# Performance work log

Measured on AMD Instinct MI355X. Metric: run time of the kernel, lower is better.

## Reference

```python
import jax, jax.numpy as jnp
import numpy as np
from jax import lax
from jax.scipy.special import logsumexp

NUM_TAGS = 5
B, L = 16384, 512


def setup_inputs() -> dict:
    key = jax.random.key(0)
    k1, k2, k3, k4, k5 = jax.random.split(key, 5)
    emissions = jax.random.normal(k1, (B, L, NUM_TAGS), dtype=jnp.float32)
    tags = jax.random.randint(k2, (B, L), 0, NUM_TAGS)
    mask = jnp.ones((B, L), dtype=bool)
    # learned CRF parameters, init U(-0.1, 0.1) as in reset_parameters
    transitions = jax.random.uniform(k3, (NUM_TAGS, NUM_TAGS), minval=-0.1, maxval=0.1, dtype=jnp.float32)
    start_transitions = jax.random.uniform(k4, (NUM_TAGS,), minval=-0.1, maxval=0.1, dtype=jnp.float32)
    end_transitions = jax.random.uniform(k5, (NUM_TAGS,), minval=-0.1, maxval=0.1, dtype=jnp.float32)
    return {
        "emissions": emissions,
        "transitions": transitions,
        "start_transitions": start_transitions,
        "end_transitions": end_transitions,
        "tags": tags,
        "mask": mask,
    }


def reference(emissions, transitions, start_transitions, end_transitions, tags, mask):
    """CRF mean negative log-likelihood: log_partition - gold_score (both batch means)."""
    Bs, Ls, C = emissions.shape
    maskf = mask.astype(emissions.dtype)

    # ---- log partition (forward algorithm); note: original torch code's
    # mask application here is a no-op (where(mask, s, s)), reproduced faithfully.
    init_score = start_transitions[None, :] + emissions[:, 0]  # (B, C)

    def step(score, em_i):
        # score: (B, C) over previous tag; em_i: (B, C)
        nxt = logsumexp(score[:, :, None] + transitions[None, :, :] + em_i[:, None, :], axis=1)
        return nxt, None

    ems = jnp.swapaxes(emissions[:, 1:], 0, 1)  # (L-1, B, C)
    final_score, _ = lax.scan(step, init_score, ems)
    log_den = logsumexp(final_score + end_transitions[None, :], axis=1).mean()

    # ---- gold path score (fully vectorized over time)
    s0 = start_transitions[tags[:, 0]] + jnp.take_along_axis(emissions[:, 0], tags[:, :1], axis=1)[:, 0]
    trans_scores = transitions[tags[:, :-1], tags[:, 1:]]  # (B, L-1)
    em_at_tags = jnp.take_along_axis(emissions, tags[:, :, None], axis=2)[:, :, 0]  # (B, L)
    path_score = s0 + ((trans_scores + em_at_tags[:, 1:]) * maskf[:, 1:]).sum(axis=1)
    last_idx = mask.sum(axis=1).astype(jnp.int32) - 1  # (B,)
    last_tags = jnp.take_along_axis(tags, last_idx[:, None], axis=1)[:, 0]
    log_num = (path_score + end_transitions[last_tags]).mean()

    return log_den - log_num
```

## Files before the change

### kernel.cpp

```cpp
#include <hip/hip_runtime.h>

#define NTAGS 5
#define BATCH 16384
#define SEQL 512
#define CL 8
#define SEQF (SEQL * NTAGS)
#define PADC 41
#define SEQPF (64 * PADC)
#define PTAG 9
#define SEQPT (64 * PTAG)

__device__ __forceinline__ float sel5v(float a0, float a1, float a2, float a3, float a4, int t) {
    float r = a0;
    r = (t == 1) ? a1 : r;
    r = (t == 2) ? a2 : r;
    r = (t == 3) ? a3 : r;
    r = (t == 4) ? a4 : r;
    return r;
}

__global__ __launch_bounds__(256, 2) void crf_fused(
    const float* __restrict__ emis, const float* __restrict__ trans,
    const float* __restrict__ startT, const float* __restrict__ endT,
    const int* __restrict__ tags, float* __restrict__ out) {
    __shared__ float lemis[4 * SEQPF];
    __shared__ int ltags[4 * SEQPT];
    __shared__ float ldsT[25];
    __shared__ float lred[4];

    const int tid = threadIdx.x;
    const int lane = tid & 63;
    const int wid = tid >> 6;

    const float4* ge = (const float4*)(emis + (size_t)blockIdx.x * 4 * SEQF);
#pragma unroll
    for (int w = 0; w < 10; ++w) {
        const int f = w * 256 + tid;
        const float4 v = ge[f];
        const int F = 4 * f;
        const int s = F / SEQF;
        const int r = F - s * SEQF;
        const int piece = r / 40;
        const int off = r - piece * 40;
        float* dst = &lemis[s * SEQPF + piece * PADC + off];
        dst[0] = v.x; dst[1] = v.y; dst[2] = v.z; dst[3] = v.w;
    }
    const int4* gt4 = (const int4*)(tags + (size_t)blockIdx.x * 4 * SEQL);
#pragma unroll
    for (int w = 0; w < 2; ++w) {
        const int g = w * 256 + tid;
        const int4 v = gt4[g];
        const int T = 4 * g;
        const int s = T >> 9;
        const int q = T & 511;
        const int piece = q >> 3;
        const int j = q & 7;
        int* dst = &ltags[s * SEQPT + piece * PTAG + j];
        dst[0] = v.x; dst[1] = v.y; dst[2] = v.z; dst[3] = v.w;
    }
    if (tid < 25) ldsT[tid] = trans[tid];
    __syncthreads();

    float eT[25];
#pragma unroll
    for (int i = 0; i < 25; ++i) eT[i] = __expf(trans[i]);

    const float* E = &lemis[wid * SEQPF + lane * PADC];
    const int* G = &ltags[wid * SEQPT + lane * PTAG];

    float M[25];
#pragma unroll
    for (int i = 0; i < 25; ++i) M[i] = 0.f;
    M[0] = M[6] = M[12] = M[18] = M[24] = 1.f;
    float logS = 0.f, path = 0.f;
    int prev = (lane == 0) ? 0 : G[7 - PTAG];

#pragma unroll
    for (int t = 0; t < CL; ++t) {
        const float e0 = E[t * 5 + 0], e1 = E[t * 5 + 1], e2 = E[t * 5 + 2],
                    e3 = E[t * 5 + 3], e4 = E[t * 5 + 4];
        const int tag = G[t];
        if (lane == 0 && t == 0) {
            path += sel5v(startT[0], startT[1], startT[2], startT[3], startT[4], tag) +
                    sel5v(e0, e1, e2, e3, e4, tag);
            prev = tag;
        } else {
            const float ex0 = __expf(e0), ex1 = __expf(e1), ex2 = __expf(e2),
                        ex3 = __expf(e3), ex4 = __expf(e4);
#pragma unroll
            for (int i = 0; i < 5; ++i) {
                const float m0 = M[i * 5 + 0], m1 = M[i * 5 + 1], m2 = M[i * 5 + 2],
                            m3 = M[i * 5 + 3], m4 = M[i * 5 + 4];
#pragma unroll
                for (int j = 0; j < 5; ++j) {
                    float a = m0 * eT[j];
                    a = fmaf(m1, eT[5 + j], a);
                    a = fmaf(m2, eT[10 + j], a);
                    a = fmaf(m3, eT[15 + j], a);
                    a = fmaf(m4, eT[20 + j], a);
                    const float exj = (j == 0) ? ex0 : (j == 1) ? ex1 : (j == 2) ? ex2
                                     : (j == 3) ? ex3 : ex4;
                    M[i * 5 + j] = a * exj;
                }
            }
            path += ldsT[prev * 5 + tag] + sel5v(e0, e1, e2, e3, e4, tag);
            prev = tag;
        }
        if ((t & 3) == 3) {
            float m = M[0];
#pragma unroll
            for (int i = 1; i < 25; ++i) m = fmaxf(m, M[i]);
            logS += __logf(m);
            const float rc = __builtin_amdgcn_rcpf(m);
#pragma unroll
            for (int i = 0; i < 25; ++i) M[i] *= rc;
        }
    }

#pragma unroll
    for (int lvl = 0; lvl < 6; ++lvl) {
        const int mk = 1 << lvl;
        float O[25];
#pragma unroll
        for (int i = 0; i < 25; ++i) O[i] = __shfl_xor(M[i], mk, 64);
        const float oS = __shfl_xor(logS, mk, 64);
        const bool hi = (lane & mk) != 0;
        float L[25], R[25];
#pragma unroll
        for (int i = 0; i < 25; ++i) {
            L[i] = hi ? O[i] : M[i];
            R[i] = hi ? M[i] : O[i];
        }
        float NM[25];
#pragma unroll
        for (int i = 0; i < 5; ++i)
#pragma unroll
            for (int j = 0; j < 5; ++j) {
                float a = L[i * 5 + 0] * R[0 * 5 + j];
                a = fmaf(L[i * 5 + 1], R[1 * 5 + j], a);
                a = fmaf(L[i * 5 + 2], R[2 * 5 + j], a);
                a = fmaf(L[i * 5 + 3], R[3 * 5 + j], a);
                a = fmaf(L[i * 5 + 4], R[4 * 5 + j], a);
                NM[i * 5 + j] = a;
            }
        logS += oS;
        float mx = NM[0];
#pragma unroll
        for (int i = 1; i < 25; ++i) mx = fmaxf(mx, NM[i]);
        logS += __logf(mx);
        const float rc = __builtin_amdgcn_rcpf(mx);
#pragma unroll
        for (int i = 0; i < 25; ++i) M[i] = NM[i] * rc;
    }

#pragma unroll
    for (int o = 1; o < 64; o <<= 1) path += __shfl_xor(path, o, 64);

    const float* E0 = &lemis[wid * SEQPF];
    const float s0 = startT[0] + E0[0], s1 = startT[1] + E0[1], s2 = startT[2] + E0[2],
                s3 = startT[3] + E0[3], s4 = startT[4] + E0[4];
    const float m0 = fmaxf(fmaxf(fmaxf(s0, s1), fmaxf(s2, s3)), s4);
    const float v0 = __expf(s0 - m0), v1 = __expf(s1 - m0), v2 = __expf(s2 - m0),
                v3 = __expf(s3 - m0), v4 = __expf(s4 - m0);
    float nv[5];
#pragma unroll
    for (int j = 0; j < 5; ++j) {
        float a = v0 * M[0 * 5 + j];
        a = fmaf(v1, M[1 * 5 + j], a);
        a = fmaf(v2, M[2 * 5 + j], a);
        a = fmaf(v3, M[3 * 5 + j], a);
        a = fmaf(v4, M[4 * 5 + j], a);
        nv[j] = a;
    }
    const float en0 = endT[0], en1 = endT[1], en2 = endT[2], en3 = endT[3], en4 = endT[4];
    float sden = nv[0] * __expf(en0);
    sden = fmaf(nv[1], __expf(en1), sden);
    sden = fmaf(nv[2], __expf(en2), sden);
    sden = fmaf(nv[3], __expf(en3), sden);
    sden = fmaf(nv[4], __expf(en4), sden);
    const float den = m0 + logS + __logf(sden);

    const int lastTag = ltags[wid * SEQPT + 63 * PTAG + 7];
    const float num = path + sel5v(en0, en1, en2, en3, en4, lastTag);

    const float res = (den - num) * (1.0f / (float)BATCH);
    if (lane == 0) lred[wid] = res;
    __syncthreads();
    if (tid == 0) atomicAdd(out, lred[0] + lred[1] + lred[2] + lred[3]);
}

extern "C" void kernel_launch(void* const* d_in, const int* in_sizes, int n_in,
                              void* d_out, int out_size, void* d_ws, size_t ws_size,
                              hipStream_t stream) {
    const float* emis = (const float*)d_in[0];
    const float* trans = (const float*)d_in[1];
    const float* startT = (const float*)d_in[2];
    const float* endT = (const float*)d_in[3];
    const int* tags = (const int*)d_in[4];
    float* out = (float*)d_out;

    hipMemsetAsync(out, 0, sizeof(float), stream);
    crf_fused<<<dim3(BATCH / 4), dim3(256), 0, stream>>>(emis, trans, startT, endT, tags,
                                                         out);
}
```

Baseline: 307.0 us.

## Split CRF into chunk-matrix phase and per-sequence vector combine phase

The in-wave 6-level butterfly of 5x5 matrix products is cut to 2 levels. Each group of 4 lanes writes its 5x5 transfer matrix, log scale and partial path score to a workspace, and a second kernel folds the 16 records per sequence with cheap vector-matrix products. Phase 1 also drops the first-step identity multiply by seeding M directly, normalises once instead of every 4 steps, and computes the gold path score in a separate loop. This removes most of the 125-FMA matrix-matrix products and shuffles at the cost of a workspace round trip through global memory and a second launch. Skipping normalisation inside the chunk and between the two butterfly levels risks overflow or underflow.

New measurement: 296.4 us. -3.4%, faster.

```diff
diff --git a/kernel.cpp b/kernel.cpp
--- a/kernel.cpp
+++ b/kernel.cpp
@@ -9,6 +9,8 @@
 #define SEQPF (64 * PADC)
 #define PTAG 9
 #define SEQPT (64 * PTAG)
+#define NREC 16
+#define RECF 28
 
 __device__ __forceinline__ float sel5v(float a0, float a1, float a2, float a3, float a4, int t) {
     float r = a0;
@@ -18,15 +20,17 @@
     r = (t == 4) ? a4 : r;
     return r;
 }
-
-__global__ __launch_bounds__(256, 2) void crf_fused(
+__device__ __forceinline__ float f4c(float4 v, int c) {
+    switch (c & 3) { case 0: return v.x; case 1: return v.y; case 2: return v.z; default: return v.w; }
+}
+
+__global__ __launch_bounds__(256, 2) void crf_phase1(
     const float* __restrict__ emis, const float* __restrict__ trans,
-    const float* __restrict__ startT, const float* __restrict__ endT,
-    const int* __restrict__ tags, float* __restrict__ out) {
+    const float* __restrict__ startT, const int* __restrict__ tags,
+    float* __restrict__ ws) {
     __shared__ float lemis[4 * SEQPF];
     __shared__ int ltags[4 * SEQPT];
     __shared__ float ldsT[25];
-    __shared__ float lred[4];
 
     const int tid = threadIdx.x;
     const int lane = tid & 63;
@@ -64,29 +68,50 @@
     float eT[25];
 #pragma unroll
     for (int i = 0; i < 25; ++i) eT[i] = __expf(trans[i]);
+    float stR[5];
+#pragma unroll
+    for (int j = 0; j < 5; ++j) stR[j] = startT[j];
 
     const float* E = &lemis[wid * SEQPF + lane * PADC];
     const int* G = &ltags[wid * SEQPT + lane * PTAG];
 
+    float path = 0.f;
+    int prev = (lane == 0) ? 0 : G[7 - PTAG];
+#pragma unroll
+    for (int t = 0; t < CL; ++t) {
+        const int tag = G[t];
+        const float et = E[t * 5 + tag];
+        if (lane == 0 && t == 0) {
+            path += sel5v(stR[0], stR[1], stR[2], stR[3], stR[4], tag) + et;
+        } else {
+            path += ldsT[prev * 5 + tag] + et;
+        }
+        prev = tag;
+    }
+
     float M[25];
-#pragma unroll
-    for (int i = 0; i < 25; ++i) M[i] = 0.f;
-    M[0] = M[6] = M[12] = M[18] = M[24] = 1.f;
-    float logS = 0.f, path = 0.f;
-    int prev = (lane == 0) ? 0 : G[7 - PTAG];
-
-#pragma unroll
-    for (int t = 0; t < CL; ++t) {
-        const float e0 = E[t * 5 + 0], e1 = E[t * 5 + 1], e2 = E[t * 5 + 2],
-                    e3 = E[t * 5 + 3], e4 = E[t * 5 + 4];
-        const int tag = G[t];
-        if (lane == 0 && t == 0) {
-            path += sel5v(startT[0], startT[1], startT[2], startT[3], startT[4], tag) +
-                    sel5v(e0, e1, e2, e3, e4, tag);
-            prev = tag;
-        } else {
-            const float ex0 = __expf(e0), ex1 = __expf(e1), ex2 = __expf(e2),
-                        ex3 = __expf(e3), ex4 = __expf(e4);
+    float logS = 0.f;
+    const int bump = (lane == 0) ? 1 : 0;
+    {
+        const float* e = &E[bump * 5];
+        const float x0 = __expf(e[0]), x1 = __expf(e[1]), x2 = __expf(e[2]),
+                    x3 = __expf(e[3]), x4 = __expf(e[4]);
+#pragma unroll
+        for (int i = 0; i < 5; ++i) {
+            M[i * 5 + 0] = eT[i * 5 + 0] * x0;
+            M[i * 5 + 1] = eT[i * 5 + 1] * x1;
+            M[i * 5 + 2] = eT[i * 5 + 2] * x2;
+            M[i * 5 + 3] = eT[i * 5 + 3] * x3;
+            M[i * 5 + 4] = eT[i * 5 + 4] * x4;
+        }
+    }
+#pragma unroll
+    for (int u = 1; u < CL; ++u) {
+        const int s = u + bump;
+        if (s < CL) {
+            const float* e = &E[s * 5];
+            const float ex0 = __expf(e[0]), ex1 = __expf(e[1]), ex2 = __expf(e[2]),
+                        ex3 = __expf(e[3]), ex4 = __expf(e[4]);
 #pragma unroll
             for (int i = 0; i < 5; ++i) {
                 const float m0 = M[i * 5 + 0], m1 = M[i * 5 + 1], m2 = M[i * 5 + 2],
@@ -103,22 +128,20 @@
                     M[i * 5 + j] = a * exj;
                 }
             }
-            path += ldsT[prev * 5 + tag] + sel5v(e0, e1, e2, e3, e4, tag);
-            prev = tag;
-        }
-        if ((t & 3) == 3) {
-            float m = M[0];
-#pragma unroll
-            for (int i = 1; i < 25; ++i) m = fmaxf(m, M[i]);
-            logS += __logf(m);
-            const float rc = __builtin_amdgcn_rcpf(m);
-#pragma unroll
-            for (int i = 0; i < 25; ++i) M[i] *= rc;
-        }
-    }
-
-#pragma unroll
-    for (int lvl = 0; lvl < 6; ++lvl) {
+        }
+    }
+    {
+        float mx = M[0];
+#pragma unroll
+        for (int i = 1; i < 25; ++i) mx = fmaxf(mx, M[i]);
+        logS += __logf(mx);
+        const float rc = __builtin_amdgcn_rcpf(mx);
+#pragma unroll
+        for (int i = 0; i < 25; ++i) M[i] *= rc;
+    }
+
+#pragma unroll
+    for (int lvl = 0; lvl < 2; ++lvl) {
         const int mk = 1 << lvl;
         float O[25];
 #pragma unroll
@@ -131,7 +154,6 @@
             L[i] = hi ? O[i] : M[i];
             R[i] = hi ? M[i] : O[i];
         }
-        float NM[25];
 #pragma unroll
         for (int i = 0; i < 5; ++i)
 #pragma unroll
@@ -141,52 +163,118 @@
                 a = fmaf(L[i * 5 + 2], R[2 * 5 + j], a);
                 a = fmaf(L[i * 5 + 3], R[3 * 5 + j], a);
                 a = fmaf(L[i * 5 + 4], R[4 * 5 + j], a);
-                NM[i * 5 + j] = a;
+                M[i * 5 + j] = a;
             }
         logS += oS;
-        float mx = NM[0];
-#pragma unroll
-        for (int i = 1; i < 25; ++i) mx = fmaxf(mx, NM[i]);
+    }
+    {
+        float mx = M[0];
+#pragma unroll
+        for (int i = 1; i < 25; ++i) mx = fmaxf(mx, M[i]);
         logS += __logf(mx);
         const float rc = __builtin_amdgcn_rcpf(mx);
 #pragma unroll
-        for (int i = 0; i < 25; ++i) M[i] = NM[i] * rc;
-    }
-
-#pragma unroll
-    for (int o = 1; o < 64; o <<= 1) path += __shfl_xor(path, o, 64);
-
-    const float* E0 = &lemis[wid * SEQPF];
-    const float s0 = startT[0] + E0[0], s1 = startT[1] + E0[1], s2 = startT[2] + E0[2],
-                s3 = startT[3] + E0[3], s4 = startT[4] + E0[4];
+        for (int i = 0; i < 25; ++i) M[i] *= rc;
+    }
+    path += __shfl_xor(path, 1, 64);
+    path += __shfl_xor(path, 2, 64);
+
+    float* rb = &lemis[wid * SEQPF];
+    if ((lane & 3) == 0) {
+        float* r = &rb[(lane >> 2) * RECF];
+#pragma unroll
+        for (int i = 0; i < 25; ++i) r[i] = M[i];
+        r[25] = logS;
+        r[26] = path;
+        r[27] = 0.f;
+    }
+    __syncthreads();
+    float4* wdst = (float4*)(ws + (size_t)blockIdx.x * (4 * NREC * RECF));
+    {
+        const int F = 4 * tid;
+        const int s = F / 448;
+        const int r = F - s * 448;
+        wdst[tid] = *(const float4*)&lemis[s * SEQPF + r];
+        if (tid < 192) {
+            const int k = 256 + tid;
+            const int F2 = 4 * k;
+            const int s2 = F2 / 448;
+            const int r2 = F2 - s2 * 448;
+            wdst[k] = *(const float4*)&lemis[s2 * SEQPF + r2];
+        }
+    }
+}
+
+__device__ __forceinline__ void p2_combine(const float4 r[7], float v[5], float& logZ,
+                                           float& path) {
+#define MM(i, j) f4c(r[((i) * 5 + (j)) >> 2], ((i) * 5 + (j)) & 3)
+    float nv[5];
+#pragma unroll
+    for (int j = 0; j < 5; ++j) {
+        float a = v[0] * MM(0, j);
+        a = fmaf(v[1], MM(1, j), a);
+        a = fmaf(v[2], MM(2, j), a);
+        a = fmaf(v[3], MM(3, j), a);
+        a = fmaf(v[4], MM(4, j), a);
+        nv[j] = a;
+    }
+#undef MM
+    logZ += r[6].y;
+    path += r[6].z;
+    const float m = fmaxf(fmaxf(fmaxf(nv[0], nv[1]), fmaxf(nv[2], nv[3])), nv[4]);
+    logZ += __logf(m);
+    const float rc = __builtin_amdgcn_rcpf(m);
+#pragma unroll
+    for (int j = 0; j < 5; ++j) v[j] = nv[j] * rc;
+}
+
+__global__ __launch_bounds__(64) void crf_phase2(
+    const float* __restrict__ emis, const float* __restrict__ startT,
+    const float* __restrict__ endT, const int* __restrict__ tags,
+    const float* __restrict__ ws, float* __restrict__ out) {
+    const int seq = blockIdx.x * 64 + threadIdx.x;
+    const float* eb = emis + (size_t)seq * (SEQL * NTAGS);
+    const float4* wsb = (const float4*)(ws + (size_t)seq * NREC * RECF);
+
+    float4 r[4][7];
+#pragma unroll
+    for (int s = 0; s < 4; ++s)
+#pragma unroll
+        for (int k = 0; k < 7; ++k) r[s][k] = wsb[s * 7 + k];
+
+    const float4 e03 = *(const float4*)eb;
+    const float e4v = eb[4];
+    const float s0 = startT[0] + e03.x, s1 = startT[1] + e03.y, s2 = startT[2] + e03.z,
+                s3 = startT[3] + e03.w, s4 = startT[4] + e4v;
     const float m0 = fmaxf(fmaxf(fmaxf(s0, s1), fmaxf(s2, s3)), s4);
-    const float v0 = __expf(s0 - m0), v1 = __expf(s1 - m0), v2 = __expf(s2 - m0),
-                v3 = __expf(s3 - m0), v4 = __expf(s4 - m0);
-    float nv[5];
-#pragma unroll
-    for (int j = 0; j < 5; ++j) {
-        float a = v0 * M[0 * 5 + j];
-        a = fmaf(v1, M[1 * 5 + j], a);
-        a = fmaf(v2, M[2 * 5 + j], a);
-        a = fmaf(v3, M[3 * 5 + j], a);
-        a = fmaf(v4, M[4 * 5 + j], a);
-        nv[j] = a;
-    }
+    float v[5] = {__expf(s0 - m0), __expf(s1 - m0), __expf(s2 - m0), __expf(s3 - m0),
+                  __expf(s4 - m0)};
+    float logZ = m0, path = 0.f;
+
+#pragma unroll
+    for (int c = 0; c < NREC; ++c) {
+        p2_combine(r[c & 3], v, logZ, path);
+        if (c + 4 < NREC) {
+#pragma unroll
+            for (int k = 0; k < 7; ++k) r[c & 3][k] = wsb[(c + 4) * 7 + k];
+        }
+    }
+
     const float en0 = endT[0], en1 = endT[1], en2 = endT[2], en3 = endT[3], en4 = endT[4];
-    float sden = nv[0] * __expf(en0);
-    sden = fmaf(nv[1], __expf(en1), sden);
-    sden = fmaf(nv[2], __expf(en2), sden);
-    sden = fmaf(nv[3], __expf(en3), sden);
-    sden = fmaf(nv[4], __expf(en4), sden);
-    const float den = m0 + logS + __logf(sden);
-
-    const int lastTag = ltags[wid * SEQPT + 63 * PTAG + 7];
+    float sden = v[0] * __expf(en0);
+    sden = fmaf(v[1], __expf(en1), sden);
+    sden = fmaf(v[2], __expf(en2), sden);
+    sden = fmaf(v[3], __expf(en3), sden);
+    sden = fmaf(v[4], __expf(en4), sden);
+    const float den = logZ + __logf(sden);
+
+    const int lastTag = tags[seq * SEQL + (SEQL - 1)];
     const float num = path + sel5v(en0, en1, en2, en3, en4, lastTag);
 
-    const float res = (den - num) * (1.0f / (float)BATCH);
-    if (lane == 0) lred[wid] = res;
-    __syncthreads();
-    if (tid == 0) atomicAdd(out, lred[0] + lred[1] + lred[2] + lred[3]);
+    float val = (den - num) * (1.0f / (float)BATCH);
+#pragma unroll
+    for (int off = 32; off > 0; off >>= 1) val += __shfl_xor(val, off, 64);
+    if (threadIdx.x == 0) atomicAdd(out, val);
 }
 
 extern "C" void kernel_launch(void* const* d_in, const int* in_sizes, int n_in,
@@ -198,8 +286,10 @@
     const float* endT = (const float*)d_in[3];
     const int* tags = (const int*)d_in[4];
     float* out = (float*)d_out;
+    float* ws = (float*)d_ws;
 
     hipMemsetAsync(out, 0, sizeof(float), stream);
-    crf_fused<<<dim3(BATCH / 4), dim3(256), 0, stream>>>(emis, trans, startT, endT, tags,
-                                                         out);
-}
+    crf_phase1<<<dim3(BATCH / 4), dim3(256), 0, stream>>>(emis, trans, startT, tags, ws);
+    crf_phase2<<<dim3(BATCH / 64), dim3(64), 0, stream>>>(emis, startT, endT, tags, ws,
+                                                          out);
+}
```

## Replace per-lane 5x5 matrix scan with forward-backward vector recurrences per sequence

Applied to the files above, without the earlier changes.

Each sequence was split into 64 chunks, each lane built a 5x5 transfer matrix with 25-element products, and the chunks were combined by a shuffle tree. The new kernel gives one thread a whole sequence half: wave 0 runs the forward recurrence over the first 256 steps and wave 1 runs the backward recurrence over the last 256. Both carry only 5-element vectors and meet at the middle through LDS. This cuts per-step arithmetic roughly fivefold and removes the matrix-combine tree. In exchange, each thread's serial chain now spans 256 steps. To hide load latency, emissions and tags are staged in 16-step windows with register prefetch and LDS double buffering, and the grid drops to 256 blocks of 128 threads, which may leave the GPU's compute units underused.

New measurement: 283.2 us. 7.8% less time.

```diff
diff --git a/kernel.cpp b/kernel.cpp
--- a/kernel.cpp
+++ b/kernel.cpp
@@ -3,12 +3,10 @@
 #define NTAGS 5
 #define BATCH 16384
 #define SEQL 512
-#define CL 8
-#define SEQF (SEQL * NTAGS)
-#define PADC 41
-#define SEQPF (64 * PADC)
-#define PTAG 9
-#define SEQPT (64 * PTAG)
+#define TW 16
+#define NW 16
+#define ROWF 81
+#define ROWT 17
 
 __device__ __forceinline__ float sel5v(float a0, float a1, float a2, float a3, float a4, int t) {
     float r = a0;
@@ -19,174 +17,201 @@
     return r;
 }
 
-__global__ __launch_bounds__(256, 2) void crf_fused(
+__global__ __launch_bounds__(128, 1) void crf_fb(
     const float* __restrict__ emis, const float* __restrict__ trans,
     const float* __restrict__ startT, const float* __restrict__ endT,
     const int* __restrict__ tags, float* __restrict__ out) {
-    __shared__ float lemis[4 * SEQPF];
-    __shared__ int ltags[4 * SEQPT];
+    __shared__ float lem[2][128 * ROWF];
+    __shared__ int ltg[2][128 * ROWT];
     __shared__ float ldsT[25];
-    __shared__ float lred[4];
+    __shared__ float xch[64][9];
 
     const int tid = threadIdx.x;
-    const int lane = tid & 63;
-    const int wid = tid >> 6;
-
-    const float4* ge = (const float4*)(emis + (size_t)blockIdx.x * 4 * SEQF);
-#pragma unroll
-    for (int w = 0; w < 10; ++w) {
-        const int f = w * 256 + tid;
-        const float4 v = ge[f];
-        const int F = 4 * f;
-        const int s = F / SEQF;
-        const int r = F - s * SEQF;
-        const int piece = r / 40;
-        const int off = r - piece * 40;
-        float* dst = &lemis[s * SEQPF + piece * PADC + off];
-        dst[0] = v.x; dst[1] = v.y; dst[2] = v.z; dst[3] = v.w;
-    }
-    const int4* gt4 = (const int4*)(tags + (size_t)blockIdx.x * 4 * SEQL);
-#pragma unroll
-    for (int w = 0; w < 2; ++w) {
-        const int g = w * 256 + tid;
-        const int4 v = gt4[g];
-        const int T = 4 * g;
-        const int s = T >> 9;
-        const int q = T & 511;
-        const int piece = q >> 3;
-        const int j = q & 7;
-        int* dst = &ltags[s * SEQPT + piece * PTAG + j];
-        dst[0] = v.x; dst[1] = v.y; dst[2] = v.z; dst[3] = v.w;
-    }
-    if (tid < 25) ldsT[tid] = trans[tid];
+    const int l = tid & 63;
+    const int wv = tid >> 6;
+    const int seqbase = blockIdx.x * 64;
+    const int lrow = wv * 64 + l;
+
+    if (l < 25) ldsT[l] = trans[l];
+
+    float eT[25];
+#pragma unroll
+    for (int i = 0; i < 25; ++i) eT[i] = __expf(trans[i]);
+    float stR[5], enT[5];
+#pragma unroll
+    for (int j = 0; j < 5; ++j) { stR[j] = startT[j]; enT[j] = endT[j]; }
+
+    const float4* ge = (const float4*)emis;
+    const int4* gt = (const int4*)tags;
+
+    float4 ev[20];
+    int4 tv[4];
+
+#define STAGE_LOAD(w_)                                                        \
+    {                                                                         \
+        const int offE = wv ? (620 - 20 * (w_)) : (20 * (w_));                \
+        const int offT = wv ? (124 - 4 * (w_)) : (4 * (w_));                  \
+        _Pragma("unroll") for (int m = 0; m < 20; ++m) {                      \
+            const int f = m * 64 + l;                                         \
+            const int r = f / 20;                                             \
+            const int k = f - r * 20;                                         \
+            ev[m] = ge[(size_t)(seqbase + r) * 640 + offE + k];               \
+        }                                                                     \
+        _Pragma("unroll") for (int m = 0; m < 4; ++m) {                       \
+            const int f = m * 64 + l;                                         \
+            tv[m] = gt[(size_t)(seqbase + (f >> 2)) * 128 + offT + (f & 3)];  \
+        }                                                                     \
+    }
+
+#define STAGE_WRITE(buf_)                                                     \
+    {                                                                         \
+        _Pragma("unroll") for (int m = 0; m < 20; ++m) {                      \
+            const int f = m * 64 + l;                                         \
+            const int r = f / 20;                                             \
+            const int k = f - r * 20;                                         \
+            float* d = &lem[buf_][(wv * 64 + r) * ROWF + 4 * k];              \
+            d[0] = ev[m].x; d[1] = ev[m].y; d[2] = ev[m].z; d[3] = ev[m].w;   \
+        }                                                                     \
+        _Pragma("unroll") for (int m = 0; m < 4; ++m) {                       \
+            const int f = m * 64 + l;                                         \
+            int* d = &ltg[buf_][(wv * 64 + (f >> 2)) * ROWT + 4 * (f & 3)];   \
+            d[0] = tv[m].x; d[1] = tv[m].y; d[2] = tv[m].z; d[3] = tv[m].w;   \
+        }                                                                     \
+    }
+
+#define RESCALE()                                                             \
+    {                                                                         \
+        const float mx =                                                      \
+            fmaxf(fmaxf(fmaxf(S[0], S[1]), fmaxf(S[2], S[3])), S[4]);         \
+        logS += __logf(mx);                                                   \
+        const float rc = __builtin_amdgcn_rcpf(mx);                           \
+        S[0] *= rc; S[1] *= rc; S[2] *= rc; S[3] *= rc; S[4] *= rc;           \
+    }
+
+    STAGE_LOAD(0)
+    STAGE_WRITE(0)
+    STAGE_LOAD(1)
+    asm volatile("s_waitcnt lgkmcnt(0)" ::: "memory");
+    __builtin_amdgcn_sched_barrier(0);
+
+    float S[5];
+    float logS = 0.f, path = 0.f;
+    int carry = 0, lastTag = 0;
+    if (wv == 1) {
+#pragma unroll
+        for (int j = 0; j < 5; ++j) S[j] = __expf(enT[j]);
+    }
+
+#pragma unroll 1
+    for (int w = 0; w < NW; ++w) {
+        const float* E = &lem[w & 1][lrow * ROWF];
+        const int* G = &ltg[w & 1][lrow * ROWT];
+        if (wv == 0) {
+#pragma unroll
+            for (int u = 0; u < TW; ++u) {
+                const float e0 = E[u * 5 + 0], e1 = E[u * 5 + 1], e2 = E[u * 5 + 2],
+                            e3 = E[u * 5 + 3], e4 = E[u * 5 + 4];
+                const int tag = G[u];
+                const float esel = sel5v(e0, e1, e2, e3, e4, tag);
+                if (u == 0 && w == 0) {
+                    S[0] = __expf(stR[0] + e0); S[1] = __expf(stR[1] + e1);
+                    S[2] = __expf(stR[2] + e2); S[3] = __expf(stR[3] + e3);
+                    S[4] = __expf(stR[4] + e4);
+                    path = sel5v(stR[0], stR[1], stR[2], stR[3], stR[4], tag) + esel;
+                } else {
+                    const float ex0 = __expf(e0), ex1 = __expf(e1), ex2 = __expf(e2),
+                                ex3 = __expf(e3), ex4 = __expf(e4);
+                    float n0 = S[0] * eT[0];
+                    n0 = fmaf(S[1], eT[5], n0);  n0 = fmaf(S[2], eT[10], n0);
+                    n0 = fmaf(S[3], eT[15], n0); n0 = fmaf(S[4], eT[20], n0); n0 *= ex0;
+                    float n1 = S[0] * eT[1];
+                    n1 = fmaf(S[1], eT[6], n1);  n1 = fmaf(S[2], eT[11], n1);
+                    n1 = fmaf(S[3], eT[16], n1); n1 = fmaf(S[4], eT[21], n1); n1 *= ex1;
+                    float n2 = S[0] * eT[2];
+                    n2 = fmaf(S[1], eT[7], n2);  n2 = fmaf(S[2], eT[12], n2);
+                    n2 = fmaf(S[3], eT[17], n2); n2 = fmaf(S[4], eT[22], n2); n2 *= ex2;
+                    float n3 = S[0] * eT[3];
+                    n3 = fmaf(S[1], eT[8], n3);  n3 = fmaf(S[2], eT[13], n3);
+                    n3 = fmaf(S[3], eT[18], n3); n3 = fmaf(S[4], eT[23], n3); n3 *= ex3;
+                    float n4 = S[0] * eT[4];
+                    n4 = fmaf(S[1], eT[9], n4);  n4 = fmaf(S[2], eT[14], n4);
+                    n4 = fmaf(S[3], eT[19], n4); n4 = fmaf(S[4], eT[24], n4); n4 *= ex4;
+                    path += ldsT[carry * 5 + tag] + esel;
+                    S[0] = n0; S[1] = n1; S[2] = n2; S[3] = n3; S[4] = n4;
+                }
+                carry = tag;
+                if (u == 7 || u == 15) RESCALE()
+            }
+        } else {
+            int tcur = G[15];
+#pragma unroll
+            for (int uu = 0; uu < TW; ++uu) {
+                const int u = 15 - uu;
+                const float e0 = E[u * 5 + 0], e1 = E[u * 5 + 1], e2 = E[u * 5 + 2],
+                            e3 = E[u * 5 + 3], e4 = E[u * 5 + 4];
+                const int tag = tcur;
+                const float g0 = __expf(e0) * S[0], g1 = __expf(e1) * S[1],
+                            g2 = __expf(e2) * S[2], g3 = __expf(e3) * S[3],
+                            g4 = __expf(e4) * S[4];
+                float n0 = g0 * eT[0];
+                n0 = fmaf(g1, eT[1], n0);  n0 = fmaf(g2, eT[2], n0);
+                n0 = fmaf(g3, eT[3], n0);  n0 = fmaf(g4, eT[4], n0);
+                float n1 = g0 * eT[5];
+                n1 = fmaf(g1, eT[6], n1);  n1 = fmaf(g2, eT[7], n1);
+                n1 = fmaf(g3, eT[8], n1);  n1 = fmaf(g4, eT[9], n1);
+                float n2 = g0 * eT[10];
+                n2 = fmaf(g1, eT[11], n2); n2 = fmaf(g2, eT[12], n2);
+                n2 = fmaf(g3, eT[13], n2); n2 = fmaf(g4, eT[14], n2);
+                float n3 = g0 * eT[15];
+                n3 = fmaf(g1, eT[16], n3); n3 = fmaf(g2, eT[17], n3);
+                n3 = fmaf(g3, eT[18], n3); n3 = fmaf(g4, eT[19], n3);
+                float n4 = g0 * eT[20];
+                n4 = fmaf(g1, eT[21], n4); n4 = fmaf(g2, eT[22], n4);
+                n4 = fmaf(g3, eT[23], n4); n4 = fmaf(g4, eT[24], n4);
+                path += sel5v(e0, e1, e2, e3, e4, tag);
+                if (u == 15) {
+                    if (w == 0) lastTag = tag;
+                    else path += ldsT[tag * 5 + carry];
+                }
+                if (u >= 1) {
+                    const int tprev = G[u - 1];
+                    path += ldsT[tprev * 5 + tag];
+                    tcur = tprev;
+                } else {
+                    carry = tag;
+                }
+                S[0] = n0; S[1] = n1; S[2] = n2; S[3] = n3; S[4] = n4;
+                if (u == 8 || u == 0) RESCALE()
+            }
+        }
+        if (w + 1 < NW) {
+            STAGE_WRITE((w + 1) & 1)
+            if (w + 2 < NW) STAGE_LOAD(w + 2)
+            asm volatile("s_waitcnt lgkmcnt(0)" ::: "memory");
+            __builtin_amdgcn_sched_barrier(0);
+        }
+    }
+
+    if (wv == 0) {
+        float* x = xch[l];
+        x[0] = S[0]; x[1] = S[1]; x[2] = S[2]; x[3] = S[3]; x[4] = S[4];
+        x[5] = logS; x[6] = path; x[7] = __int_as_float(carry);
+    }
     __syncthreads();
-
-    float eT[25];
-#pragma unroll
-    for (int i = 0; i < 25; ++i) eT[i] = __expf(trans[i]);
-
-    const float* E = &lemis[wid * SEQPF + lane * PADC];
-    const int* G = &ltags[wid * SEQPT + lane * PTAG];
-
-    float M[25];
-#pragma unroll
-    for (int i = 0; i < 25; ++i) M[i] = 0.f;
-    M[0] = M[6] = M[12] = M[18] = M[24] = 1.f;
-    float logS = 0.f, path = 0.f;
-    int prev = (lane == 0) ? 0 : G[7 - PTAG];
-
-#pragma unroll
-    for (int t = 0; t < CL; ++t) {
-        const float e0 = E[t * 5 + 0], e1 = E[t * 5 + 1], e2 = E[t * 5 + 2],
-                    e3 = E[t * 5 + 3], e4 = E[t * 5 + 4];
-        const int tag = G[t];
-        if (lane == 0 && t == 0) {
-            path += sel5v(startT[0], startT[1], startT[2], startT[3], startT[4], tag) +
-                    sel5v(e0, e1, e2, e3, e4, tag);
-            prev = tag;
-        } else {
-            const float ex0 = __expf(e0), ex1 = __expf(e1), ex2 = __expf(e2),
-                        ex3 = __expf(e3), ex4 = __expf(e4);
-#pragma unroll
-            for (int i = 0; i < 5; ++i) {
-                const float m0 = M[i * 5 + 0], m1 = M[i * 5 + 1], m2 = M[i * 5 + 2],
-                            m3 = M[i * 5 + 3], m4 = M[i * 5 + 4];
-#pragma unroll
-                for (int j = 0; j < 5; ++j) {
-                    float a = m0 * eT[j];
-                    a = fmaf(m1, eT[5 + j], a);
-                    a = fmaf(m2, eT[10 + j], a);
-                    a = fmaf(m3, eT[15 + j], a);
-                    a = fmaf(m4, eT[20 + j], a);
-                    const float exj = (j == 0) ? ex0 : (j == 1) ? ex1 : (j == 2) ? ex2
-                                     : (j == 3) ? ex3 : ex4;
-                    M[i * 5 + j] = a * exj;
-                }
-            }
-            path += ldsT[prev * 5 + tag] + sel5v(e0, e1, e2, e3, e4, tag);
-            prev = tag;
-        }
-        if ((t & 3) == 3) {
-            float m = M[0];
-#pragma unroll
-            for (int i = 1; i < 25; ++i) m = fmaxf(m, M[i]);
-            logS += __logf(m);
-            const float rc = __builtin_amdgcn_rcpf(m);
-#pragma unroll
-            for (int i = 0; i < 25; ++i) M[i] *= rc;
-        }
-    }
-
-#pragma unroll
-    for (int lvl = 0; lvl < 6; ++lvl) {
-        const int mk = 1 << lvl;
-        float O[25];
-#pragma unroll
-        for (int i = 0; i < 25; ++i) O[i] = __shfl_xor(M[i], mk, 64);
-        const float oS = __shfl_xor(logS, mk, 64);
-        const bool hi = (lane & mk) != 0;
-        float L[25], R[25];
-#pragma unroll
-        for (int i = 0; i < 25; ++i) {
-            L[i] = hi ? O[i] : M[i];
-            R[i] = hi ? M[i] : O[i];
-        }
-        float NM[25];
-#pragma unroll
-        for (int i = 0; i < 5; ++i)
-#pragma unroll
-            for (int j = 0; j < 5; ++j) {
-                float a = L[i * 5 + 0] * R[0 * 5 + j];
-                a = fmaf(L[i * 5 + 1], R[1 * 5 + j], a);
-                a = fmaf(L[i * 5 + 2], R[2 * 5 + j], a);
-                a = fmaf(L[i * 5 + 3], R[3 * 5 + j], a);
-                a = fmaf(L[i * 5 + 4], R[4 * 5 + j], a);
-                NM[i * 5 + j] = a;
-            }
-        logS += oS;
-        float mx = NM[0];
-#pragma unroll
-        for (int i = 1; i < 25; ++i) mx = fmaxf(mx, NM[i]);
-        logS += __logf(mx);
-        const float rc = __builtin_amdgcn_rcpf(mx);
-#pragma unroll
-        for (int i = 0; i < 25; ++i) M[i] = NM[i] * rc;
-    }
-
-#pragma unroll
-    for (int o = 1; o < 64; o <<= 1) path += __shfl_xor(path, o, 64);
-
-    const float* E0 = &lemis[wid * SEQPF];
-    const float s0 = startT[0] + E0[0], s1 = startT[1] + E0[1], s2 = startT[2] + E0[2],
-                s3 = startT[3] + E0[3], s4 = startT[4] + E0[4];
-    const float m0 = fmaxf(fmaxf(fmaxf(s0, s1), fmaxf(s2, s3)), s4);
-    const float v0 = __expf(s0 - m0), v1 = __expf(s1 - m0), v2 = __expf(s2 - m0),
-                v3 = __expf(s3 - m0), v4 = __expf(s4 - m0);
-    float nv[5];
-#pragma unroll
-    for (int j = 0; j < 5; ++j) {
-        float a = v0 * M[0 * 5 + j];
-        a = fmaf(v1, M[1 * 5 + j], a);
-        a = fmaf(v2, M[2 * 5 + j], a);
-        a = fmaf(v3, M[3 * 5 + j], a);
-        a = fmaf(v4, M[4 * 5 + j], a);
-        nv[j] = a;
-    }
-    const float en0 = endT[0], en1 = endT[1], en2 = endT[2], en3 = endT[3], en4 = endT[4];
-    float sden = nv[0] * __expf(en0);
-    sden = fmaf(nv[1], __expf(en1), sden);
-    sden = fmaf(nv[2], __expf(en2), sden);
-    sden = fmaf(nv[3], __expf(en3), sden);
-    sden = fmaf(nv[4], __expf(en4), sden);
-    const float den = m0 + logS + __logf(sden);
-
-    const int lastTag = ltags[wid * SEQPT + 63 * PTAG + 7];
-    const float num = path + sel5v(en0, en1, en2, en3, en4, lastTag);
-
-    const float res = (den - num) * (1.0f / (float)BATCH);
-    if (lane == 0) lred[wid] = res;
-    __syncthreads();
-    if (tid == 0) atomicAdd(out, lred[0] + lred[1] + lred[2] + lred[3]);
+    if (wv == 1) {
+        const float* x = xch[l];
+        float s = x[0] * S[0];
+        s = fmaf(x[1], S[1], s); s = fmaf(x[2], S[2], s);
+        s = fmaf(x[3], S[3], s); s = fmaf(x[4], S[4], s);
+        const float den = __logf(s) + x[5] + logS;
+        const int t255 = __float_as_int(x[7]);
+        const float num = x[6] + path + ldsT[t255 * 5 + carry] +
+                          sel5v(enT[0], enT[1], enT[2], enT[3], enT[4], lastTag);
+        float val = (den - num) * (1.0f / (float)BATCH);
+#pragma unroll
+        for (int o = 1; o < 64; o <<= 1) val += __shfl_xor(val, o, 64);
+        if (l == 0) atomicAdd(out, val);
+    }
 }
 
 extern "C" void kernel_launch(void* const* d_in, const int* in_sizes, int n_in,
@@ -200,6 +225,6 @@
     float* out = (float*)d_out;
 
     hipMemsetAsync(out, 0, sizeof(float), stream);
-    crf_fused<<<dim3(BATCH / 4), dim3(256), 0, stream>>>(emis, trans, startT, endT, tags,
-                                                         out);
+    crf_fb<<<dim3(BATCH / 64), dim3(128), 0, stream>>>(emis, trans, startT, endT, tags,
+                                                       out);
 }
```
